# Performance work log

Measured on AMD Instinct MI355X. Metric: run time of the kernel, lower is better.

Reference implementation:

```python
import jax, jax.numpy as jnp
import numpy as np

B, S, D, H = 2, 2048, 1024, 16
HD = D // H
WIN = 32
LN_EPS = 1e-5


def _ln(x, g, b):
    m = jnp.mean(x, axis=-1, keepdims=True)
    v = jnp.mean(jnp.square(x - m), axis=-1, keepdims=True)
    return (x - m) / jnp.sqrt(v + LN_EPS) * g + b


def setup_inputs() -> dict:
    key = jax.random.key(0)
    ks = jax.random.split(key, 12)
    def w(k, shape):
        return jax.random.normal(k, shape, dtype=jnp.float32) * 0.02
    inp = {
        'x': jax.random.normal(ks[0], (B, S, D), dtype=jnp.float32),
        'fq_w': w(ks[1], (D, D)), 'fq_b': jnp.zeros((D,), jnp.float32),
        'fk_w': w(ks[2], (D, D)), 'fk_b': jnp.zeros((D,), jnp.float32),
        'fv_w': w(ks[3], (D, D)), 'fv_b': jnp.zeros((D,), jnp.float32),
        'bq_w': w(ks[4], (D, D)), 'bq_b': jnp.zeros((D,), jnp.float32),
        'bk_w': w(ks[5], (D, D)), 'bk_b': jnp.zeros((D,), jnp.float32),
        'bv_w': w(ks[6], (D, D)), 'bv_b': jnp.zeros((D,), jnp.float32),
        'gate_w': w(ks[7], (2 * D, D)), 'gate_b': jnp.zeros((D,), jnp.float32),
        'gln_g': jnp.ones((D,), jnp.float32), 'gln_b': jnp.zeros((D,), jnp.float32),
        'bstr': jnp.asarray(0.1, jnp.float32),
        'out_w': w(ks[8], (D, D)), 'out_b': jnp.zeros((D,), jnp.float32),
        'ln_g': jnp.ones((D,), jnp.float32), 'ln_b': jnp.zeros((D,), jnp.float32),
    }
    return inp


def _heads(x, w, b):
    # [B,S,D] -> [B,H,S,HD]
    y = x @ w + b
    return y.reshape(B, S, H, HD).transpose(0, 2, 1, 3)


def _merge(x):
    return x.transpose(0, 2, 1, 3).reshape(B, S, D)


def _forward(x, fq_w, fq_b, fk_w, fk_b, fv_w, fv_b,
             bq_w, bq_b, bk_w, bk_b, bv_w, bv_b,
             gate_w, gate_b, gln_g, gln_b, bstr, out_w, out_b, ln_g, ln_b):
    scale = 1.0 / np.sqrt(HD)
    i = jnp.arange(S)
    # --- causal forward attention ---
    Q = _heads(x, fq_w, fq_b); K = _heads(x, fk_w, fk_b); V = _heads(x, fv_w, fv_b)
    scores = jnp.einsum('bhqd,bhkd->bhqk', Q, K) * scale
    causal = i[:, None] >= i[None, :]  # allowed positions
    scores = jnp.where(causal[None, None], scores, -jnp.inf)
    fwd = _merge(jnp.einsum('bhqk,bhkd->bhqd', jax.nn.softmax(scores, axis=-1), V))
    # --- limited-window backward attention (future_context = hidden_states) ---
    Qb = _heads(x, bq_w, bq_b); Kb = _heads(x, bk_w, bk_b); Vb = _heads(x, bv_w, bv_b)
    sb = jnp.einsum('bhqd,bhkd->bhqk', Qb, Kb) * scale
    valid = (i[None, :] > i[:, None]) & (i[None, :] <= i[:, None] + WIN)
    sb = jnp.where(valid[None, None], sb, -jnp.inf)
    # rows with no valid future (last row) get scores reset to 0 -> uniform softmax,
    # matching torch's all_masked handling
    row_valid = valid.any(axis=-1)  # [S]
    sb = jnp.where(row_valid[None, None, :, None], sb, 0.0)
    bwd = _merge(jnp.einsum('bhqk,bhkd->bhqd', jax.nn.softmax(sb, axis=-1), Vb))
    # --- weak gated fusion (eval mode: no dropout, backward detached) ---
    combined = jnp.concatenate([fwd, bwd], axis=-1)
    gate = jax.nn.sigmoid(_ln(combined @ gate_w + gate_b, gln_g, gln_b))
    strength = jax.nn.sigmoid(bstr) * 0.3
    fused = fwd + strength * gate * jax.lax.stop_gradient(bwd)
    out = fused @ out_w + out_b
    return _ln(x + out, ln_g, ln_b)


def reference(x, fq_w, fq_b, fk_w, fk_b, fv_w, fv_b,
              bq_w, bq_b, bk_w, bk_b, bv_w, bv_b,
              gate_w, gate_b, gln_g, gln_b, bstr, out_w, out_b, ln_g, ln_b):
    return _forward(x, fq_w, fq_b, fk_w, fk_b, fv_w, fv_b,
                    bq_w, bq_b, bk_w, bk_b, bv_w, bv_b,
                    gate_w, gate_b, gln_g, gln_b, bstr, out_w, out_b, ln_g, ln_b)
```

## Files before the change

### kernel.cpp

```cpp
#include <hip/hip_runtime.h>

#define S_LEN 2048
#define NH 16
#define HD 64
#define DMODEL 1024
#define NTOK 4096
#define ELTS_PER 4194304
#define QSCALE 0.18033688f

typedef __attribute__((ext_vector_type(8))) __bf16 bfrag;
typedef __attribute__((ext_vector_type(8))) short s8v;
typedef __attribute__((ext_vector_type(4))) float f32x4;

__device__ inline float bf2f(short s) {
  unsigned int u = ((unsigned int)(unsigned short)s) << 16;
  float f;
  __builtin_memcpy(&f, &u, 4);
  return f;
}
__device__ inline short f2bf(float f) {
  unsigned int u;
  __builtin_memcpy(&u, &f, 4);
  u = (u + 0x7fffu + ((u >> 16) & 1u)) >> 16;
  return (short)u;
}
__device__ inline short f2bf_n(float f) {
  __bf16 h = (__bf16)f;
  short s;
  __builtin_memcpy(&s, &h, 2);
  return s;
}
__device__ inline float bflo(unsigned int u) {
  unsigned int t = u << 16;
  float f; __builtin_memcpy(&f, &t, 4); return f;
}
__device__ inline float bfhi(unsigned int u) {
  unsigned int t = u & 0xffff0000u;
  float f; __builtin_memcpy(&f, &t, 4); return f;
}
__device__ __forceinline__ void gll16(const short* g, short* l) {
  __builtin_amdgcn_global_load_lds(
      (const __attribute__((address_space(1))) void*)g,
      (__attribute__((address_space(3))) void*)l, 16, 0, 0);
}

__global__ __launch_bounds__(256) void cvt_bf16_kernel(const float* __restrict__ in,
                                                       short* __restrict__ out, int n) {
  int i = (blockIdx.x * 256 + threadIdx.x) * 4;
  if (i + 3 < n) {
    float4 v = *reinterpret_cast<const float4*>(in + i);
    short4 o;
    o.x = f2bf(v.x); o.y = f2bf(v.y); o.z = f2bf(v.z); o.w = f2bf(v.w);
    *reinterpret_cast<short4*>(out + i) = o;
  }
}

__global__ void transpose_cvt_all(const float* __restrict__ s0, const float* __restrict__ s1,
                                  const float* __restrict__ s2, const float* __restrict__ s3,
                                  const float* __restrict__ s4, const float* __restrict__ s5,
                                  const float* __restrict__ s6, const float* __restrict__ s7,
                                  short* d0, short* d1, short* d2, short* d3,
                                  short* d4, short* d5, short* d6, short* d7) {
  const int z = blockIdx.z;
  const int K = (z == 7) ? 2048 : 1024;
  if (blockIdx.y * 32 >= K) return;
  const float* srcs[8] = {s0, s1, s2, s3, s4, s5, s6, s7};
  short* dsts[8] = {d0, d1, d2, d3, d4, d5, d6, d7};
  const float* in = srcs[z];
  short* out = dsts[z];
  __shared__ float tile[32][33];
  int nb = blockIdx.x * 32, kb = blockIdx.y * 32;
  int tx = threadIdx.x, ty = threadIdx.y;
  for (int j = 0; j < 32; j += 8)
    tile[ty + j][tx] = in[(size_t)(kb + ty + j) * 1024 + nb + tx];
  __syncthreads();
  for (int j = 0; j < 32; j += 8)
    out[(size_t)(nb + ty + j) * K + kb + tx] = f2bf(tile[tx][ty + j]);
}

__global__ __launch_bounds__(256) void gemm_qkv_kernel(
    const short* __restrict__ A, int lda, int K,
    const short* __restrict__ B0, const short* __restrict__ B1, const short* __restrict__ B2,
    const short* __restrict__ B3, const short* __restrict__ B4, const short* __restrict__ B5,
    const float* __restrict__ bias0, const float* __restrict__ bias1,
    const float* __restrict__ bias2, const float* __restrict__ bias3,
    const float* __restrict__ bias4, const float* __restrict__ bias5,
    short* __restrict__ outQ) {
  __shared__ short lds[128 * 136];
  short* As = lds;
  short* Bs = lds + 8192;
  const int tid = threadIdx.x;
  const int n0 = blockIdx.x * 128;
  const int m0 = blockIdx.y * 128;
  const short* Bp[6] = {B0, B1, B2, B3, B4, B5};
  const float* biasP[6] = {bias0, bias1, bias2, bias3, bias4, bias5};
  const int nsel = n0 >> 10;
  const int nc0 = n0 & 1023;
  const short* Bt = Bp[nsel] + (size_t)nc0 * K;
  const float* bsel = biasP[nsel];

  const int lane = tid & 63;
  const int w = tid >> 6;
  const int wm = (w >> 1) * 64;
  const int wn = (w & 1) * 64;
  const int lr = lane & 15;
  const int lg = lane >> 4;
  const int rl = lane >> 3;
  const int gch = (lane & 7) ^ (rl & 7);

  f32x4 acc[4][4];
  for (int a = 0; a < 4; ++a)
    for (int b = 0; b < 4; ++b) acc[a][b] = {0.f, 0.f, 0.f, 0.f};

  for (int k0 = 0; k0 < K; k0 += 64) {
    __syncthreads();
    for (int p = 0; p < 4; ++p) {
      int rb = (p * 4 + w) * 8;
      gll16(A + (size_t)(m0 + rb + rl) * lda + k0 + gch * 8, &As[rb * 64]);
      gll16(Bt + (size_t)(rb + rl) * K + k0 + gch * 8, &Bs[rb * 64]);
    }
    __syncthreads();
    for (int ks = 0; ks < 2; ++ks) {
      bfrag af[4], bf[4];
      for (int t = 0; t < 4; ++t) {
        af[t] = *reinterpret_cast<const bfrag*>(
            &As[(wm + t * 16 + lr) * 64 + (((lg + 4 * ks) ^ (lr & 7)) * 8)]);
        bf[t] = *reinterpret_cast<const bfrag*>(
            &Bs[(wn + t * 16 + lr) * 64 + (((lg + 4 * ks) ^ (lr & 7)) * 8)]);
      }
      for (int mt = 0; mt < 4; ++mt)
        for (int nt = 0; nt < 4; ++nt)
          acc[mt][nt] = __builtin_amdgcn_mfma_f32_16x16x32_bf16(af[mt], bf[nt], acc[mt][nt], 0, 0, 0);
    }
  }

  const float cmul = (nsel == 0 || nsel == 3) ? QSCALE : 1.0f;
  const bool tr = (nsel == 2 || nsel == 5);
  __syncthreads();
  for (int mt = 0; mt < 4; ++mt)
    for (int nt = 0; nt < 4; ++nt) {
      int c = wn + nt * 16 + lr;
      float bv = bsel[nc0 + c];
      for (int i = 0; i < 4; ++i) {
        int r = wm + mt * 16 + lg * 4 + i;
        short v16 = f2bf_n((acc[mt][nt][i] + bv) * cmul);
        if (tr) lds[c * 136 + r] = v16;
        else lds[r * 136 + c] = v16;
      }
    }
  __syncthreads();
  const int bb = m0 >> 11;
  const int sloc = m0 & 2047;
  const int hh0 = nc0 >> 6;
  short* basebuf = outQ + (size_t)nsel * ELTS_PER;
  for (int j = 0; j < 8; ++j) {
    int gid = j * 256 + tid;
    int rr = gid >> 4;
    int ch = gid & 15;
    s8v v = *reinterpret_cast<const s8v*>(&lds[rr * 136 + ch * 8]);
    if (tr) {
      int hh = hh0 + (rr >> 6), d = rr & 63;
      *reinterpret_cast<s8v*>(
          basebuf + ((size_t)(bb * NH + hh) * HD + d) * S_LEN + sloc + ch * 8) = v;
    } else {
      int hh = hh0 + (ch >> 3), d0 = (ch & 7) * 8;
      *reinterpret_cast<s8v*>(
          basebuf + ((size_t)(bb * NH + hh) * S_LEN + sloc + rr) * HD + d0) = v;
    }
  }
}

__global__ __launch_bounds__(256) void gemm_ksplit_kernel(
    const short* __restrict__ A0, const short* __restrict__ A1, int lda,
    const short* __restrict__ B, int ldb, int K,
    const float* __restrict__ bias, float* __restrict__ out0, float* __restrict__ out1) {
  __shared__ short lds[16384];
  short* As = lds;
  short* Bs = lds + 8192;
  const int tid = threadIdx.x;
  const int n0 = blockIdx.x * 128;
  const int m0 = blockIdx.y * 128;
  const int z = blockIdx.z;
  const short* A = z ? A1 : A0;
  const short* Bt = B + (size_t)n0 * ldb + z * K;
  float* outp = z ? out1 : out0;

  const int lane = tid & 63;
  const int w = tid >> 6;
  const int wm = (w >> 1) * 64;
  const int wn = (w & 1) * 64;
  const int lr = lane & 15;
  const int lg = lane >> 4;
  const int rl = lane >> 3;
  const int gch = (lane & 7) ^ (rl & 7);

  f32x4 acc[4][4];
  for (int a = 0; a < 4; ++a)
    for (int b = 0; b < 4; ++b) acc[a][b] = {0.f, 0.f, 0.f, 0.f};

  for (int k0 = 0; k0 < K; k0 += 64) {
    __syncthreads();
    for (int p = 0; p < 4; ++p) {
      int rb = (p * 4 + w) * 8;
      gll16(A + (size_t)(m0 + rb + rl) * lda + k0 + gch * 8, &As[rb * 64]);
      gll16(Bt + (size_t)(rb + rl) * ldb + k0 + gch * 8, &Bs[rb * 64]);
    }
    __syncthreads();
    for (int ks = 0; ks < 2; ++ks) {
      bfrag af[4], bf[4];
      for (int t = 0; t < 4; ++t) {
        af[t] = *reinterpret_cast<const bfrag*>(
            &As[(wm + t * 16 + lr) * 64 + (((lg + 4 * ks) ^ (lr & 7)) * 8)]);
        bf[t] = *reinterpret_cast<const bfrag*>(
            &Bs[(wn + t * 16 + lr) * 64 + (((lg + 4 * ks) ^ (lr & 7)) * 8)]);
      }
      for (int mt = 0; mt < 4; ++mt)
        for (int nt = 0; nt < 4; ++nt)
          acc[mt][nt] = __builtin_amdgcn_mfma_f32_16x16x32_bf16(af[mt], bf[nt], acc[mt][nt], 0, 0, 0);
    }
  }

  for (int mt = 0; mt < 4; ++mt)
    for (int nt = 0; nt < 4; ++nt)
      for (int i = 0; i < 4; ++i) {
        int row = m0 + wm + mt * 16 + lg * 4 + i;
        int col = n0 + wn + nt * 16 + lr;
        float v = acc[mt][nt][i] + (z == 0 ? bias[col] : 0.f);
        outp[(size_t)row * DMODEL + col] = v;
      }
}

__global__ __launch_bounds__(256) void attn_fwd_kernel(const short* __restrict__ Q,
                                                       const short* __restrict__ Kk,
                                                       const short* __restrict__ VT,
                                                       short* __restrict__ fwd) {
  __shared__ short Ps[4][32 * 72];
  const int tid = threadIdx.x;
  const int lane = tid & 63;
  const int w = tid >> 6;
  const int lr = lane & 15;
  const int lg = lane >> 4;
  const int f = blockIdx.x;
  const int xcd = f & 7;
  const int slot = f >> 3;
  const int bh = xcd * 4 + (slot >> 4);
  const int p = slot & 15;
  const int b = bh >> 4;
  const int h = bh & 15;
  const size_t hb = (size_t)(b * NH + h) * S_LEN * HD;
  short* Pw = Ps[w];

  s8v onesi = {0x3F80, 0x3F80, 0x3F80, 0x3F80, 0x3F80, 0x3F80, 0x3F80, 0x3F80};
  bfrag onesv;
  __builtin_memcpy(&onesv, &onesi, 16);

  const int c = (w < 2) ? (2 * p + w) : (63 - 2 * p - (w - 2));
  const int q0 = c * 32;
  const int ktm = c >> 1;

  bfrag qf[2][2];
  for (int mt = 0; mt < 2; ++mt)
    for (int kc = 0; kc < 2; ++kc)
      qf[mt][kc] = *reinterpret_cast<const bfrag*>(
          Q + hb + (size_t)(q0 + mt * 16 + lr) * HD + kc * 32 + lg * 8);

  f32x4 oacc[2][4];
  for (int mt = 0; mt < 2; ++mt)
    for (int nd = 0; nd < 4; ++nd) oacc[mt][nd] = {0.f, 0.f, 0.f, 0.f};
  f32x4 osum[2];
  osum[0] = {0.f, 0.f, 0.f, 0.f};
  osum[1] = {0.f, 0.f, 0.f, 0.f};

  bfrag ka0[4][2], ka1[4][2];
  for (int nb = 0; nb < 4; ++nb)
    for (int kc = 0; kc < 2; ++kc)
      ka0[nb][kc] = *reinterpret_cast<const bfrag*>(
          Kk + hb + (size_t)(nb * 16 + lr) * HD + kc * 32 + lg * 8);

#define FWD_BODY(KCUR, KNXT)                                                        \
  do {                                                                              \
    if (kt < ktm) {                                                                 \
      for (int nb = 0; nb < 4; ++nb)                                                \
        for (int kc = 0; kc < 2; ++kc)                                              \
          KNXT[nb][kc] = *reinterpret_cast<const bfrag*>(                           \
              Kk + hb + (size_t)((kt + 1) * 64 + nb * 16 + lr) * HD + kc * 32 +     \
              lg * 8);                                                              \
    }                                                                               \
    bfrag vf[4][2];                                                                 \
    for (int nd = 0; nd < 4; ++nd)                                                  \
      for (int kc = 0; kc < 2; ++kc)                                                \
        vf[nd][kc] = *reinterpret_cast<const bfrag*>(                               \
            VT + hb + (size_t)(nd * 16 + lr) * S_LEN + kt * 64 + kc * 32 + lg * 8); \
    f32x4 sv[2][4];                                                                 \
    for (int mt = 0; mt < 2; ++mt)                                                  \
      for (int nb = 0; nb < 4; ++nb) {                                              \
        f32x4 z = {0.f, 0.f, 0.f, 0.f};                                             \
        z = __builtin_amdgcn_mfma_f32_16x16x32_bf16(qf[mt][0], KCUR[nb][0], z, 0, 0, 0); \
        sv[mt][nb] =                                                                \
            __builtin_amdgcn_mfma_f32_16x16x32_bf16(qf[mt][1], KCUR[nb][1], z, 0, 0, 0); \
      }                                                                             \
    if (kt == ktm) {                                                                \
      for (int mt = 0; mt < 2; ++mt)                                                \
        for (int nb = 0; nb < 4; ++nb)                                              \
          for (int i = 0; i < 4; ++i) {                                             \
            int colg = kt * 64 + nb * 16 + lr;                                      \
            int rowg = q0 + mt * 16 + lg * 4 + i;                                   \
            if (colg > rowg) sv[mt][nb][i] = -1e30f;                                \
          }                                                                         \
    }                                                                               \
    for (int mt = 0; mt < 2; ++mt)                                                  \
      for (int nb = 0; nb < 4; ++nb)                                                \
        for (int i = 0; i < 4; ++i)                                                 \
          Pw[(mt * 16 + lg * 4 + i) * 72 + nb * 16 + lr] =                          \
              f2bf_n(exp2f(sv[mt][nb][i]));                                         \
    for (int mt = 0; mt < 2; ++mt) {                                                \
      bfrag pa0 = *reinterpret_cast<const bfrag*>(&Pw[(mt * 16 + lr) * 72 + lg * 8]); \
      bfrag pa1 =                                                                   \
          *reinterpret_cast<const bfrag*>(&Pw[(mt * 16 + lr) * 72 + 32 + lg * 8]);  \
      for (int nd = 0; nd < 4; ++nd) {                                              \
        oacc[mt][nd] =                                                              \
            __builtin_amdgcn_mfma_f32_16x16x32_bf16(pa0, vf[nd][0], oacc[mt][nd], 0, 0, 0); \
        oacc[mt][nd] =                                                              \
            __builtin_amdgcn_mfma_f32_16x16x32_bf16(pa1, vf[nd][1], oacc[mt][nd], 0, 0, 0); \
      }                                                                             \
      osum[mt] = __builtin_amdgcn_mfma_f32_16x16x32_bf16(pa0, onesv, osum[mt], 0, 0, 0); \
      osum[mt] = __builtin_amdgcn_mfma_f32_16x16x32_bf16(pa1, onesv, osum[mt], 0, 0, 0); \
    }                                                                               \
  } while (0)

  for (int kt = 0; kt <= ktm; ++kt) {
    if ((kt & 1) == 0) FWD_BODY(ka0, ka1);
    else FWD_BODY(ka1, ka0);
  }
#undef FWD_BODY

  for (int mt = 0; mt < 2; ++mt)
    for (int i = 0; i < 4; ++i) {
      int rowg = q0 + mt * 16 + lg * 4 + i;
      float inv = 1.0f / osum[mt][i];
      for (int nd = 0; nd < 4; ++nd)
        fwd[(size_t)(b * S_LEN + rowg) * DMODEL + h * HD + nd * 16 + lr] =
            f2bf(oacc[mt][nd][i] * inv);
    }
}

__global__ __launch_bounds__(256) void attn_bwd_kernel(const short* __restrict__ Qb,
                                                       const short* __restrict__ Kb,
                                                       const short* __restrict__ VT,
                                                       short* __restrict__ bwd) {
  __shared__ short Ps[4][32 * 72];
  const int tid = threadIdx.x;
  const int lane = tid & 63;
  const int w = tid >> 6;
  const int lr = lane & 15;
  const int lg = lane >> 4;
  const int h = blockIdx.y;
  const int b = blockIdx.z;
  const size_t hb = (size_t)(b * NH + h) * S_LEN * HD;
  const int q0 = blockIdx.x * 128 + w * 32;
  short* Pw = Ps[w];

  bfrag qf[2][2];
  for (int mt = 0; mt < 2; ++mt)
    for (int kc = 0; kc < 2; ++kc)
      qf[mt][kc] = *reinterpret_cast<const bfrag*>(
          Qb + hb + (size_t)(q0 + mt * 16 + lr) * HD + kc * 32 + lg * 8);
  bfrag kf[4][2];
  for (int nb = 0; nb < 4; ++nb) {
    int kr = q0 + nb * 16 + lr;
    kr = min(kr, S_LEN - 1);
    for (int kc = 0; kc < 2; ++kc)
      kf[nb][kc] = *reinterpret_cast<const bfrag*>(
          Kb + hb + (size_t)kr * HD + kc * 32 + lg * 8);
  }
  f32x4 sv[2][4];
  for (int mt = 0; mt < 2; ++mt)
    for (int nb = 0; nb < 4; ++nb) {
      f32x4 z = {0.f, 0.f, 0.f, 0.f};
      z = __builtin_amdgcn_mfma_f32_16x16x32_bf16(qf[mt][0], kf[nb][0], z, 0, 0, 0);
      sv[mt][nb] = __builtin_amdgcn_mfma_f32_16x16x32_bf16(qf[mt][1], kf[nb][1], z, 0, 0, 0);
    }
  float mx[2][4];
  for (int mt = 0; mt < 2; ++mt)
    for (int i = 0; i < 4; ++i) {
      int rowg = q0 + mt * 16 + lg * 4 + i;
      float m = -1e30f;
      for (int nb = 0; nb < 4; ++nb) {
        int colg = q0 + nb * 16 + lr;
        float t = sv[mt][nb][i];
        bool valid = (colg > rowg) && (colg <= rowg + 32) && (colg < S_LEN);
        if (!valid) t = -1e30f;
        sv[mt][nb][i] = t;
        m = fmaxf(m, t);
      }
      mx[mt][i] = m;
    }
  for (int off = 1; off < 16; off <<= 1)
    for (int mt = 0; mt < 2; ++mt)
      for (int i = 0; i < 4; ++i) mx[mt][i] = fmaxf(mx[mt][i], __shfl_xor(mx[mt][i], off));
  float rs[2][4] = {{0.f, 0.f, 0.f, 0.f}, {0.f, 0.f, 0.f, 0.f}};
  for (int mt = 0; mt < 2; ++mt)
    for (int nb = 0; nb < 4; ++nb)
      for (int i = 0; i < 4; ++i) {
        float p = exp2f(sv[mt][nb][i] - mx[mt][i]);
        rs[mt][i] += p;
        Pw[(mt * 16 + lg * 4 + i) * 72 + nb * 16 + lr] = f2bf_n(p);
      }
  for (int off = 1; off < 16; off <<= 1)
    for (int mt = 0; mt < 2; ++mt)
      for (int i = 0; i < 4; ++i) rs[mt][i] += __shfl_xor(rs[mt][i], off);
  bfrag vf[4][2];
  for (int nd = 0; nd < 4; ++nd)
    for (int kc = 0; kc < 2; ++kc) {
      int sbase = q0 + kc * 32 + lg * 8;
      sbase = min(sbase, S_LEN - 8);
      vf[nd][kc] = *reinterpret_cast<const bfrag*>(
          VT + hb + (size_t)(nd * 16 + lr) * S_LEN + sbase);
    }
  f32x4 oacc[2][4];
  for (int mt = 0; mt < 2; ++mt)
    for (int nd = 0; nd < 4; ++nd) oacc[mt][nd] = {0.f, 0.f, 0.f, 0.f};
  for (int mt = 0; mt < 2; ++mt) {
    bfrag pa0 = *reinterpret_cast<const bfrag*>(&Pw[(mt * 16 + lr) * 72 + lg * 8]);
    bfrag pa1 = *reinterpret_cast<const bfrag*>(&Pw[(mt * 16 + lr) * 72 + 32 + lg * 8]);
    for (int nd = 0; nd < 4; ++nd) {
      oacc[mt][nd] = __builtin_amdgcn_mfma_f32_16x16x32_bf16(pa0, vf[nd][0], oacc[mt][nd], 0, 0, 0);
      oacc[mt][nd] = __builtin_amdgcn_mfma_f32_16x16x32_bf16(pa1, vf[nd][1], oacc[mt][nd], 0, 0, 0);
    }
  }
  for (int mt = 0; mt < 2; ++mt)
    for (int nd = 0; nd < 4; ++nd)
      for (int i = 0; i < 4; ++i) {
        int rowg = q0 + mt * 16 + lg * 4 + i;
        float ov = oacc[mt][nd][i] / rs[mt][i];
        bwd[(size_t)(b * S_LEN + rowg) * DMODEL + h * HD + nd * 16 + lr] = f2bf(ov);
      }
}

__global__ __launch_bounds__(256) void vmean_kernel(const short* __restrict__ VT,
                                                    short* __restrict__ bwd) {
  __shared__ float red[256];
  const int bh = blockIdx.x;
  const int d = threadIdx.x >> 2;
  const int seg = threadIdx.x & 3;
  const short* row = VT + (size_t)bh * S_LEN * HD + (size_t)d * S_LEN + seg * 512;
  float s = 0.f;
  for (int j = 0; j < 512; j += 8) {
    uint4 v = *reinterpret_cast<const uint4*>(row + j);
    s += bflo(v.x) + bfhi(v.x) + bflo(v.y) + bfhi(v.y) +
         bflo(v.z) + bfhi(v.z) + bflo(v.w) + bfhi(v.w);
  }
  red[threadIdx.x] = s;
  __syncthreads();
  if (seg == 0) {
    float t = red[d * 4] + red[d * 4 + 1] + red[d * 4 + 2] + red[d * 4 + 3];
    int b = bh >> 4, h = bh & 15;
    bwd[((size_t)(b * S_LEN + S_LEN - 1)) * DMODEL + h * HD + d] = f2bf(t * (1.f / S_LEN));
  }
}

__global__ __launch_bounds__(256) void ln_gate_fuse_kernel(
    const float* __restrict__ g0p, const float* __restrict__ g1p,
    const float* __restrict__ gln_g, const float* __restrict__ gln_b,
    const short* __restrict__ fwd, const short* __restrict__ bwd,
    const float* __restrict__ bstr, short* __restrict__ fused) {
  __shared__ float red[8];
  const int row = blockIdx.x;
  const int tid = threadIdx.x;
  const int lane = tid & 63;
  const int w = tid >> 6;
  float4 x0 = *reinterpret_cast<const float4*>(g0p + (size_t)row * DMODEL + tid * 4);
  float4 x1 = *reinterpret_cast<const float4*>(g1p + (size_t)row * DMODEL + tid * 4);
  float xa[4] = {x0.x + x1.x, x0.y + x1.y, x0.z + x1.z, x0.w + x1.w};
  float s = xa[0] + xa[1] + xa[2] + xa[3];
  float ss = xa[0] * xa[0] + xa[1] * xa[1] + xa[2] * xa[2] + xa[3] * xa[3];
  for (int off = 1; off < 64; off <<= 1) {
    s += __shfl_xor(s, off);
    ss += __shfl_xor(ss, off);
  }
  if (lane == 0) { red[w] = s; red[4 + w] = ss; }
  __syncthreads();
  s = red[0] + red[1] + red[2] + red[3];
  ss = red[4] + red[5] + red[6] + red[7];
  const float mean = s * (1.f / DMODEL);
  const float var = ss * (1.f / DMODEL) - mean * mean;
  const float rstd = rsqrtf(var + 1e-5f);
  const float strength = 0.3f / (1.f + __expf(-bstr[0]));
  for (int e = 0; e < 4; ++e) {
    int idx = tid * 4 + e;
    float g = (xa[e] - mean) * rstd * gln_g[idx] + gln_b[idx];
    float gate = 1.f / (1.f + __expf(-g));
    float f = bf2f(fwd[(size_t)row * DMODEL + idx]) +
              strength * gate * bf2f(bwd[(size_t)row * DMODEL + idx]);
    fused[(size_t)row * DMODEL + idx] = f2bf(f);
  }
}

__global__ __launch_bounds__(256) void final_ln_kernel(const float* __restrict__ x,
                                                       const float* __restrict__ o0p,
                                                       const float* __restrict__ o1p,
                                                       const float* __restrict__ ln_g,
                                                       const float* __restrict__ ln_b,
                                                       float* __restrict__ y) {
  __shared__ float red[8];
  const int row = blockIdx.x;
  const int tid = threadIdx.x;
  const int lane = tid & 63;
  const int w = tid >> 6;
  float4 xv = *reinterpret_cast<const float4*>(x + (size_t)row * DMODEL + tid * 4);
  float4 o0 = *reinterpret_cast<const float4*>(o0p + (size_t)row * DMODEL + tid * 4);
  float4 o1 = *reinterpret_cast<const float4*>(o1p + (size_t)row * DMODEL + tid * 4);
  float t[4] = {xv.x + o0.x + o1.x, xv.y + o0.y + o1.y,
                xv.z + o0.z + o1.z, xv.w + o0.w + o1.w};
  float s = t[0] + t[1] + t[2] + t[3];
  float ss = t[0] * t[0] + t[1] * t[1] + t[2] * t[2] + t[3] * t[3];
  for (int off = 1; off < 64; off <<= 1) {
    s += __shfl_xor(s, off);
    ss += __shfl_xor(ss, off);
  }
  if (lane == 0) { red[w] = s; red[4 + w] = ss; }
  __syncthreads();
  s = red[0] + red[1] + red[2] + red[3];
  ss = red[4] + red[5] + red[6] + red[7];
  const float mean = s * (1.f / DMODEL);
  const float var = ss * (1.f / DMODEL) - mean * mean;
  const float rstd = rsqrtf(var + 1e-5f);
  for (int e = 0; e < 4; ++e) {
    int idx = tid * 4 + e;
    y[(size_t)row * DMODEL + idx] = (t[e] - mean) * rstd * ln_g[idx] + ln_b[idx];
  }
}

extern "C" void kernel_launch(void* const* d_in, const int* in_sizes, int n_in,
                              void* d_out, int out_size, void* d_ws, size_t ws_size,
                              hipStream_t stream) {
  const float* x = (const float*)d_in[0];
  const float* fq_w = (const float*)d_in[1];
  const float* fq_b = (const float*)d_in[2];
  const float* fk_w = (const float*)d_in[3];
  const float* fk_b = (const float*)d_in[4];
  const float* fv_w = (const float*)d_in[5];
  const float* fv_b = (const float*)d_in[6];
  const float* bq_w = (const float*)d_in[7];
  const float* bq_b = (const float*)d_in[8];
  const float* bk_w = (const float*)d_in[9];
  const float* bk_b = (const float*)d_in[10];
  const float* bv_w = (const float*)d_in[11];
  const float* bv_b = (const float*)d_in[12];
  const float* gate_w = (const float*)d_in[13];
  const float* gate_b = (const float*)d_in[14];
  const float* gln_g = (const float*)d_in[15];
  const float* gln_b = (const float*)d_in[16];
  const float* bstr = (const float*)d_in[17];
  const float* out_w = (const float*)d_in[18];
  const float* out_b = (const float*)d_in[19];
  const float* ln_g = (const float*)d_in[20];
  const float* ln_b = (const float*)d_in[21];

  char* ws = (char*)d_ws;
  const size_t MB = 1u << 20;
  short* xb = (short*)(ws + 0);
  short* wT0 = (short*)(ws + 8 * MB);
  short* wT1 = (short*)(ws + 10 * MB);
  short* wT2 = (short*)(ws + 12 * MB);
  short* wT3 = (short*)(ws + 14 * MB);
  short* wT4 = (short*)(ws + 16 * MB);
  short* wT5 = (short*)(ws + 18 * MB);
  short* gwT = (short*)(ws + 20 * MB);
  short* owT = (short*)(ws + 24 * MB);
  short* qkv = (short*)(ws + 26 * MB);
  short* fwd = (short*)(ws + 0);
  short* bwdb = (short*)(ws + 8 * MB);
  float* G0 = (float*)(ws + 26 * MB);
  float* G1 = (float*)(ws + 42 * MB);
  short* fused = (short*)(ws + 58 * MB);
  float* O0 = (float*)(ws + 26 * MB);
  float* O1 = (float*)(ws + 42 * MB);

  cvt_bf16_kernel<<<4096, 256, 0, stream>>>(x, xb, ELTS_PER);
  transpose_cvt_all<<<dim3(32, 64, 8), dim3(32, 8), 0, stream>>>(
      fq_w, fk_w, fv_w, bq_w, bk_w, bv_w, out_w, gate_w,
      wT0, wT1, wT2, wT3, wT4, wT5, owT, gwT);

  gemm_qkv_kernel<<<dim3(48, 32), 256, 0, stream>>>(
      xb, 1024, 1024, wT0, wT1, wT2, wT3, wT4, wT5,
      fq_b, fk_b, fv_b, bq_b, bk_b, bv_b, qkv);

  attn_fwd_kernel<<<512, 256, 0, stream>>>(
      qkv, qkv + (size_t)ELTS_PER, qkv + 2 * (size_t)ELTS_PER, fwd);
  attn_bwd_kernel<<<dim3(16, 16, 2), 256, 0, stream>>>(
      qkv + 3 * (size_t)ELTS_PER, qkv + 4 * (size_t)ELTS_PER, qkv + 5 * (size_t)ELTS_PER, bwdb);
  vmean_kernel<<<32, 256, 0, stream>>>(qkv + 5 * (size_t)ELTS_PER, bwdb);

  gemm_ksplit_kernel<<<dim3(8, 32, 2), 256, 0, stream>>>(
      fwd, bwdb, 1024, gwT, 2048, 1024, gate_b, G0, G1);

  ln_gate_fuse_kernel<<<4096, 256, 0, stream>>>(G0, G1, gln_g, gln_b, fwd, bwdb, bstr, fused);

  gemm_ksplit_kernel<<<dim3(8, 32, 2), 256, 0, stream>>>(
      fused, fused + 512, 1024, owT, 1024, 512, out_b, O0, O1);

  final_ln_kernel<<<4096, 256, 0, stream>>>(x, O0, O1, ln_g, ln_b, (float*)d_out);
}
```

Measured before the change: 267.4 us.

## Software-pipeline QK^T of the next tile behind softmax/PV in forward attention

Restructures the causal forward attention loop so the QK^T score MFMAs for tile kt+1 are issued between the exp/LDS-store of tile kt and its PV MFMAs, using double-buffered score registers and double-buffered per-wave LDS P tiles. The goal is to overlap matrix-core work with the exp and LDS traffic. In exchange it doubles the LDS footprint and raises register pressure from the extra score accumulators, which could lower occupancy.

```diff
diff --git a/kernel.cpp b/kernel.cpp
--- a/kernel.cpp
+++ b/kernel.cpp
@@ -234,7 +234,7 @@
                                                        const short* __restrict__ Kk,
                                                        const short* __restrict__ VT,
                                                        short* __restrict__ fwd) {
-  __shared__ short Ps[4][32 * 72];
+  __shared__ short Ps[4][2][32 * 72];
   const int tid = threadIdx.x;
   const int lane = tid & 63;
   const int w = tid >> 6;
@@ -248,7 +248,8 @@
   const int b = bh >> 4;
   const int h = bh & 15;
   const size_t hb = (size_t)(b * NH + h) * S_LEN * HD;
-  short* Pw = Ps[w];
+  short* P0w = &Ps[w][0][0];
+  short* P1w = &Ps[w][1][0];
 
   s8v onesi = {0x3F80, 0x3F80, 0x3F80, 0x3F80, 0x3F80, 0x3F80, 0x3F80, 0x3F80};
   bfrag onesv;
@@ -272,17 +273,25 @@
   osum[1] = {0.f, 0.f, 0.f, 0.f};
 
   bfrag ka0[4][2], ka1[4][2];
+  f32x4 svA[2][4], svB[2][4];
+
   for (int nb = 0; nb < 4; ++nb)
     for (int kc = 0; kc < 2; ++kc)
       ka0[nb][kc] = *reinterpret_cast<const bfrag*>(
           Kk + hb + (size_t)(nb * 16 + lr) * HD + kc * 32 + lg * 8);
-
-#define FWD_BODY(KCUR, KNXT)                                                        \
+  for (int mt = 0; mt < 2; ++mt)
+    for (int nb = 0; nb < 4; ++nb) {
+      f32x4 z = {0.f, 0.f, 0.f, 0.f};
+      z = __builtin_amdgcn_mfma_f32_16x16x32_bf16(qf[mt][0], ka0[nb][0], z, 0, 0, 0);
+      svA[mt][nb] = __builtin_amdgcn_mfma_f32_16x16x32_bf16(qf[mt][1], ka0[nb][1], z, 0, 0, 0);
+    }
+
+#define PHASE(SVC, SVN, KAN, PB)                                                    \
   do {                                                                              \
-    if (kt < ktm) {                                                                 \
+    if (kt + 1 <= ktm) {                                                            \
       for (int nb = 0; nb < 4; ++nb)                                                \
         for (int kc = 0; kc < 2; ++kc)                                              \
-          KNXT[nb][kc] = *reinterpret_cast<const bfrag*>(                           \
+          KAN[nb][kc] = *reinterpret_cast<const bfrag*>(                            \
               Kk + hb + (size_t)((kt + 1) * 64 + nb * 16 + lr) * HD + kc * 32 +     \
               lg * 8);                                                              \
     }                                                                               \
@@ -291,32 +300,33 @@
       for (int kc = 0; kc < 2; ++kc)                                                \
         vf[nd][kc] = *reinterpret_cast<const bfrag*>(                               \
             VT + hb + (size_t)(nd * 16 + lr) * S_LEN + kt * 64 + kc * 32 + lg * 8); \
-    f32x4 sv[2][4];                                                                 \
-    for (int mt = 0; mt < 2; ++mt)                                                  \
-      for (int nb = 0; nb < 4; ++nb) {                                              \
-        f32x4 z = {0.f, 0.f, 0.f, 0.f};                                             \
-        z = __builtin_amdgcn_mfma_f32_16x16x32_bf16(qf[mt][0], KCUR[nb][0], z, 0, 0, 0); \
-        sv[mt][nb] =                                                                \
-            __builtin_amdgcn_mfma_f32_16x16x32_bf16(qf[mt][1], KCUR[nb][1], z, 0, 0, 0); \
-      }                                                                             \
     if (kt == ktm) {                                                                \
       for (int mt = 0; mt < 2; ++mt)                                                \
         for (int nb = 0; nb < 4; ++nb)                                              \
           for (int i = 0; i < 4; ++i) {                                             \
             int colg = kt * 64 + nb * 16 + lr;                                      \
             int rowg = q0 + mt * 16 + lg * 4 + i;                                   \
-            if (colg > rowg) sv[mt][nb][i] = -1e30f;                                \
+            if (colg > rowg) SVC[mt][nb][i] = -1e30f;                               \
           }                                                                         \
     }                                                                               \
     for (int mt = 0; mt < 2; ++mt)                                                  \
       for (int nb = 0; nb < 4; ++nb)                                                \
         for (int i = 0; i < 4; ++i)                                                 \
-          Pw[(mt * 16 + lg * 4 + i) * 72 + nb * 16 + lr] =                          \
-              f2bf_n(exp2f(sv[mt][nb][i]));                                         \
+          PB[(mt * 16 + lg * 4 + i) * 72 + nb * 16 + lr] =                          \
+              f2bf_n(exp2f(SVC[mt][nb][i]));                                        \
+    if (kt + 1 <= ktm) {                                                            \
+      for (int mt = 0; mt < 2; ++mt)                                                \
+        for (int nb = 0; nb < 4; ++nb) {                                            \
+          f32x4 z = {0.f, 0.f, 0.f, 0.f};                                           \
+          z = __builtin_amdgcn_mfma_f32_16x16x32_bf16(qf[mt][0], KAN[nb][0], z, 0, 0, 0); \
+          SVN[mt][nb] =                                                             \
+              __builtin_amdgcn_mfma_f32_16x16x32_bf16(qf[mt][1], KAN[nb][1], z, 0, 0, 0); \
+        }                                                                           \
+    }                                                                               \
     for (int mt = 0; mt < 2; ++mt) {                                                \
-      bfrag pa0 = *reinterpret_cast<const bfrag*>(&Pw[(mt * 16 + lr) * 72 + lg * 8]); \
+      bfrag pa0 = *reinterpret_cast<const bfrag*>(&PB[(mt * 16 + lr) * 72 + lg * 8]); \
       bfrag pa1 =                                                                   \
-          *reinterpret_cast<const bfrag*>(&Pw[(mt * 16 + lr) * 72 + 32 + lg * 8]);  \
+          *reinterpret_cast<const bfrag*>(&PB[(mt * 16 + lr) * 72 + 32 + lg * 8]);  \
       for (int nd = 0; nd < 4; ++nd) {                                              \
         oacc[mt][nd] =                                                              \
             __builtin_amdgcn_mfma_f32_16x16x32_bf16(pa0, vf[nd][0], oacc[mt][nd], 0, 0, 0); \
@@ -329,10 +339,10 @@
   } while (0)
 
   for (int kt = 0; kt <= ktm; ++kt) {
-    if ((kt & 1) == 0) FWD_BODY(ka0, ka1);
-    else FWD_BODY(ka1, ka0);
-  }
-#undef FWD_BODY
+    if ((kt & 1) == 0) PHASE(svA, svB, ka1, P0w);
+    else PHASE(svB, svA, ka0, P1w);
+  }
+#undef PHASE
 
   for (int mt = 0; mt < 2; ++mt)
     for (int i = 0; i < 4; ++i) {
```

Result: slower. 288.8 us (+8.0%).
